# Optimization experiments

Measured on AMD Instinct MI355X. Metric: run time of the kernel, lower is better.

Reference implementation:

```python
import jax, jax.numpy as jnp
import numpy as np

B, S, D = 8, 2048, 1024
N = 256          # state_dim
H = 512          # selector_hidden
E = 8            # num_experts


def murmurhash3_finalizer(token_ids):
    # Torch code works in int64 but masks to 32 bits after each multiply and
    # values stay non-negative, so it is exactly uint32 wrapping arithmetic.
    x = token_ids.astype(jnp.uint32)
    x = x ^ (x >> 16)
    x = x * jnp.uint32(2246822507)
    x = x ^ (x >> 13)
    x = x * jnp.uint32(3266489909)
    x = x ^ (x >> 16)
    return x


def setup_inputs() -> dict:
    key = jax.random.key(0)
    ks = jax.random.split(key, 7)
    scale = 0.02
    return {
        "x": jax.random.normal(ks[0], (B, S, D), dtype=jnp.float32),
        "token_ids": jax.random.randint(ks[1], (B, S), 0, 50257, dtype=jnp.int32),
        "Win": jax.random.normal(ks[2], (E, N, D), dtype=jnp.float32) * scale,      # in_proj.weight per expert
        "Wsin": jax.random.normal(ks[3], (E, H, D), dtype=jnp.float32) * scale,     # selector_in.weight
        "Wsout": jax.random.normal(ks[4], (E, 4 * N, H), dtype=jnp.float32) * scale,  # selector_out.weight
        "Wout": jax.random.normal(ks[5], (E, D, N), dtype=jnp.float32) * scale,     # out_proj.weight
        "dparam": jnp.ones((E, N), dtype=jnp.float32),                              # per-expert d
    }


def _forward(x, Win, Wsin, Wsout, Wout, dparam, token_ids):
    b, s, d = x.shape
    e_num, n, _ = Win.shape
    routes = (murmurhash3_finalizer(token_ids) % jnp.uint32(e_num)).astype(jnp.int32)  # (B,S)

    # Per-token expert projections, selected by hash route (masked accumulation
    # over the small fixed expert count; honors per-token routing).
    u = jnp.zeros((b, s, n), x.dtype)
    a = jnp.zeros((b, s, n), x.dtype)
    bg = jnp.zeros((b, s, n), x.dtype)
    c = jnp.zeros((b, s, n), x.dtype)
    dg = jnp.zeros((b, s, n), x.dtype)
    for e in range(e_num):
        m = (routes == e)[..., None]
        u = jnp.where(m, jnp.einsum('bsd,nd->bsn', x, Win[e]), u)
        sh = jax.nn.silu(jnp.einsum('bsd,hd->bsh', x, Wsin[e]))
        sel = jnp.einsum('bsh,oh->bso', sh, Wsout[e])       # (B,S,4N)
        ar, br, cr, dr = jnp.split(sel, 4, axis=-1)
        a = jnp.where(m, jax.nn.sigmoid(ar), a)
        bg = jnp.where(m, jnp.tanh(br), bg)
        c = jnp.where(m, jnp.tanh(cr), c)
        dg = jnp.where(m, jax.nn.sigmoid(dr), dg)

    dvec = dparam[routes]              # (B,S,N) expert d param per token
    skip = dvec * dg * u               # residual term, state-independent

    bidx = jnp.arange(b)

    def step(states, inp):
        # states: (B,E,N) per-expert hidden state per batch row
        route_t, u_t, a_t, b_t, c_t, skip_t = inp
        h_prev = states[bidx, route_t]                 # (B,N)
        h = a_t * h_prev + b_t * u_t
        states = states.at[bidx, route_t].set(h)       # only routed expert updates
        y = c_t * h + skip_t
        return states, y

    xs = (routes.swapaxes(0, 1), u.swapaxes(0, 1), a.swapaxes(0, 1),
          bg.swapaxes(0, 1), c.swapaxes(0, 1), skip.swapaxes(0, 1))
    states0 = jnp.zeros((b, e_num, n), x.dtype)
    _, ys = jax.lax.scan(step, states0, xs)            # ys: (S,B,N)
    y = ys.swapaxes(0, 1)                              # (B,S,N)

    out = jnp.zeros((b, s, d), x.dtype)
    for e in range(e_num):
        m = (routes == e)[..., None]
        out = jnp.where(m, jnp.einsum('bsn,dn->bsd', y, Wout[e]), out)
    return out


def reference(x, token_ids, Win, Wsin, Wsout, Wout, dparam):
    return _forward(x, Win, Wsin, Wsout, Wout, dparam, token_ids)
```

## Files before the change

kernel.cpp:

```cpp
#include <hip/hip_runtime.h>


#define TOKS 16384
#define RPAD 16512
#define DD   1024
#define NN   256
#define HH   512
#define MAXTILES  136
#define MAXCHUNKS 576
#define CHUNK 32
#define CVTBLKS 12288

typedef short short8 __attribute__((ext_vector_type(8)));
typedef float floatx4 __attribute__((ext_vector_type(4)));
typedef _Float16 half_t;

#define AS_GLOBAL __attribute__((address_space(1)))
#define AS_LDS    __attribute__((address_space(3)))

__device__ __forceinline__ void gl_lds16(const void* g, void* l) {
    __builtin_amdgcn_global_load_lds((const AS_GLOBAL void*)g, (AS_LDS void*)l, 16, 0, 0);
}

__device__ __forceinline__ unsigned short f2bf(float f) {
    union { float f; unsigned u; } c; c.f = f;
    unsigned r = c.u + 0x7FFF + ((c.u >> 16) & 1);
    return (unsigned short)(r >> 16);
}
__device__ __forceinline__ int route_of(int token) {
    unsigned x = (unsigned)token;
    x ^= x >> 16; x *= 2246822507u; x ^= x >> 13; x *= 3266489909u; x ^= x >> 16;
    return (int)(x & 7u);
}
__device__ __forceinline__ float sigm(float v) { return 1.0f / (1.0f + __expf(-v)); }
__device__ __forceinline__ float ftanh(float v) {
    float e = __expf(2.0f * v);
    return 1.0f - 2.0f / (e + 1.0f);
}

__global__ void k_scatter(const int* __restrict__ tok,
                          int* __restrict__ perm,
                          int* __restrict__ tileE, int* __restrict__ tileS,
                          int* __restrict__ tileR,
                          int* __restrict__ cGrp, int* __restrict__ cStart,
                          int* __restrict__ cLen, int* __restrict__ gBase,
                          int* __restrict__ meta,
                          const float* __restrict__ Win, const float* __restrict__ Wsin,
                          const float* __restrict__ Wsout, const float* __restrict__ Wout,
                          unsigned short* __restrict__ W12, unsigned short* __restrict__ Wso,
                          unsigned short* __restrict__ Wo) {
    int blk = blockIdx.x, tid = threadIdx.x;
    if (blk >= 8) {
        const int C12 = 8 * 768 * 1024 / 4, CSO = 8 * 1024 * 512 / 4;
        int c = (blk - 8) * 256 + tid;
        floatx4 v; unsigned short* dst;
        if (c < C12) {
            int d = c * 4;
            int e = d / (768 * 1024);
            int rem = d - e * (768 * 1024);
            int r = rem >> 10, k = rem & 1023;
            const float* src = (r < 256) ? (Win + (((size_t)e * 256 + r) << 10) + k)
                                         : (Wsin + (((size_t)e * 512 + (r - 256)) << 10) + k);
            v = __builtin_nontemporal_load((const floatx4*)src);
            dst = W12 + d;
        } else if (c < C12 + CSO) {
            int d = (c - C12) * 4;
            v = __builtin_nontemporal_load((const floatx4*)(Wsout + d));
            dst = Wso + d;
        } else {
            int d = (c - C12 - CSO) * 4;
            v = __builtin_nontemporal_load((const floatx4*)(Wout + d));
            dst = Wo + d;
        }
        ushort4 o;
        o.x = f2bf(v[0]); o.y = f2bf(v[1]); o.z = f2bf(v[2]); o.w = f2bf(v[3]);
        *(ushort4*)dst = o;
        return;
    }
    int b = blk;
    int lane = tid & 63, w = tid >> 6;
    __shared__ int hh[8][8][32];
    __shared__ int sc[64], eoff[9], etile[9], gbs[65];
    __shared__ unsigned wsum[4][4];

    {
        int hr = tid >> 5, hs = tid & 31;
        const int* tp = tok + hr * 2048 + hs * 64;
        int hc[8] = {0,0,0,0,0,0,0,0};
        #pragma unroll 8
        for (int i = 0; i < 64; i++) hc[route_of(tp[i])]++;
        #pragma unroll
        for (int e = 0; e < 8; e++) hh[hr][e][hs] = hc[e];
    }
    int r[8];
    int myc[8] = {0,0,0,0,0,0,0,0};
    #pragma unroll
    for (int i = 0; i < 8; i++) {
        int e = route_of(tok[b * 2048 + tid * 8 + i]);
        r[i] = e; myc[e]++;
    }
    __syncthreads();
    if (tid < 64) {
        int row = tid >> 3, e = tid & 7, s = 0;
        #pragma unroll
        for (int s2 = 0; s2 < 32; s2++) s += hh[row][e][s2];
        sc[tid] = s;
    }
    __syncthreads();
    if (tid == 0) {
        int ce[8];
        for (int e = 0; e < 8; e++) {
            int s = 0;
            for (int b2 = 0; b2 < 8; b2++) s += sc[b2 * 8 + e];
            ce[e] = s;
        }
        eoff[0] = 0;
        for (int e = 0; e < 8; e++) eoff[e + 1] = eoff[e] + ce[e];
        if (b == 0) {
            etile[0] = 0;
            for (int e = 0; e < 8; e++) etile[e + 1] = etile[e] + (ce[e] + 127) / 128;
            meta[0] = etile[8];
            gbs[0] = 0;
            for (int g = 0; g < 64; g++) gbs[g + 1] = gbs[g] + (sc[g] + CHUNK - 1) / CHUNK;
            meta[1] = gbs[64];
        }
    }
    __syncthreads();
    unsigned p[4], v[4];
    #pragma unroll
    for (int k = 0; k < 4; k++) {
        p[k] = (unsigned)myc[2 * k] | ((unsigned)myc[2 * k + 1] << 16);
        v[k] = p[k];
    }
    #pragma unroll
    for (int off = 1; off < 64; off <<= 1) {
        #pragma unroll
        for (int k = 0; k < 4; k++) {
            unsigned o = __shfl_up(v[k], off, 64);
            if (lane >= off) v[k] += o;
        }
    }
    if (lane == 63) {
        #pragma unroll
        for (int k = 0; k < 4; k++) wsum[w][k] = v[k];
    }
    __syncthreads();
    unsigned add[4] = {0, 0, 0, 0};
    for (int ww = 0; ww < w; ww++)
        #pragma unroll
        for (int k = 0; k < 4; k++) add[k] += wsum[ww][k];
    int basep[8];
    #pragma unroll
    for (int e = 0; e < 8; e++) {
        int run = eoff[e];
        for (int b2 = 0; b2 < b; b2++) run += sc[b2 * 8 + e];
        unsigned ex = v[e >> 1] + add[e >> 1] - p[e >> 1];
        basep[e] = run + (int)((e & 1) ? (ex >> 16) : (ex & 0xffffu));
    }
    #pragma unroll
    for (int i = 0; i < 8; i++) {
        int e = r[i];
        perm[basep[e]++] = b * 2048 + tid * 8 + i;
    }
    if (b == 0) {
        if (tid < 8) {
            int e = tid, st = eoff[e], c = eoff[e + 1] - eoff[e], t0 = etile[e];
            for (int i = 0, k = 0; i < c; i += 128, k++) {
                tileE[t0 + k] = e; tileS[t0 + k] = st + i;
                tileR[t0 + k] = (c - i < 128) ? (c - i) : 128;
            }
        }
        if (tid < 64) {
            int g = tid, e = g & 7;
            int n = sc[g], base = gbs[g];
            int s0 = eoff[e];
            for (int b2 = 0; b2 < (g >> 3); b2++) s0 += sc[b2 * 8 + e];
            gBase[g] = base;
            for (int i = 0, c = 0; i < n; i += CHUNK, c++) {
                cGrp[base + c] = g;
                cStart[base + c] = s0 + i;
                cLen[base + c] = (n - i < CHUNK) ? (n - i) : CHUNK;
            }
        }
    }
}

__global__ void k_gather(const float* __restrict__ x, const int* __restrict__ perm,
                         unsigned short* __restrict__ Xs, unsigned short* __restrict__ SHb,
                         unsigned short* __restrict__ Yb) {
    int r = blockIdx.x, tid = threadIdx.x;
    if (r < TOKS) {
        int tok = perm[r];
        floatx4 v = __builtin_nontemporal_load(
            (const floatx4*)(x + (size_t)tok * 1024 + tid * 4));
        ushort4 o;
        o.x = f2bf(v[0]); o.y = f2bf(v[1]); o.z = f2bf(v[2]); o.w = f2bf(v[3]);
        *(ushort4*)(Xs + (size_t)r * 1024 + tid * 4) = o;
    } else {
        ushort4 z = {0, 0, 0, 0};
        *(ushort4*)(Xs + (size_t)r * 1024 + tid * 4) = z;
        if (tid < 128) *(ushort4*)(SHb + (size_t)r * 512 + tid * 4) = z;
        if (tid < 64)  *(ushort4*)(Yb + (size_t)r * 256 + tid * 4) = z;
    }
}

template<int MODE, int KD>
__global__ __launch_bounds__(256, 4)
void k_mfma(const unsigned short* __restrict__ A, const unsigned short* __restrict__ Bw,
            const int* __restrict__ perm, const float* __restrict__ dparam,
            half_t* __restrict__ Ub, unsigned short* __restrict__ SHb,
            half_t* __restrict__ Aa, half_t* __restrict__ Wg,
            half_t* __restrict__ Cc, half_t* __restrict__ Sk,
            float* __restrict__ out,
            const int* __restrict__ tileE, const int* __restrict__ tileS,
            const int* __restrict__ tileR, const int* __restrict__ meta) {
    const int mt = blockIdx.x;
    if (mt >= meta[0]) return;
    const int e = tileE[mt], pos0 = tileS[mt], rows = tileR[mt];
    const int col0 = blockIdx.y * 64;
    const int tid = threadIdx.x;
    const int w = tid >> 6, lane = tid & 63, quad = lane >> 4, l15 = lane & 15;
    const int wm = w & 1, wn = w >> 1;
    constexpr int NOUT = (MODE == 0) ? 768 : 1024;
    constexpr int NK = KD / 32;

    __shared__ unsigned short As[3][128 * 32];
    __shared__ unsigned short Bs[3][64 * 32];

    const int r0 = tid >> 2;
    const int c8s = ((tid & 3) ^ ((tid >> 3) & 3)) * 8;
    const unsigned short* ga = A + (size_t)(pos0 + r0) * KD + c8s;
    const unsigned short* gb = Bw + ((size_t)e * NOUT + col0 + r0) * KD + c8s;

    const int sq = (quad ^ ((l15 >> 1) & 3)) * 8;
    int aoff[4], boff[2];
    #pragma unroll
    for (int i = 0; i < 4; i++) aoff[i] = (wm * 64 + i * 16 + l15) * 32 + sq;
    #pragma unroll
    for (int j = 0; j < 2; j++) boff[j] = (wn * 32 + j * 16 + l15) * 32 + sq;

    floatx4 acc[4][2] = {};

    #define STAGE(buf, k0) do { \
        gl_lds16(ga + (k0),                    As[buf] + w * 512); \
        gl_lds16(ga + (size_t)64 * KD + (k0),  As[buf] + 2048 + w * 512); \
        gl_lds16(gb + (k0),                    Bs[buf] + w * 512); \
    } while (0)

    STAGE(0, 0);
    STAGE(1, 32);
    int cur = 0, pre = 2;
    for (int kt = 0; kt < NK; kt++) {
        if (kt < NK - 1) {
            asm volatile("s_waitcnt vmcnt(3)" ::: "memory");
        } else {
            asm volatile("s_waitcnt vmcnt(0)" ::: "memory");
        }
        __builtin_amdgcn_s_barrier();
        asm volatile("" ::: "memory");
        if (kt + 2 < NK) STAGE(pre, (kt + 2) * 32);
        short8 af[4], bf[2];
        #pragma unroll
        for (int i = 0; i < 4; i++) af[i] = *(const short8*)(As[cur] + aoff[i]);
        #pragma unroll
        for (int j = 0; j < 2; j++) bf[j] = *(const short8*)(Bs[cur] + boff[j]);
        __builtin_amdgcn_s_setprio(1);
        #pragma unroll
        for (int i = 0; i < 4; i++)
            #pragma unroll
            for (int j = 0; j < 2; j++)
                acc[i][j] = __builtin_amdgcn_mfma_f32_16x16x32_bf16(af[i], bf[j], acc[i][j], 0, 0, 0);
        __builtin_amdgcn_s_setprio(0);
        asm volatile("s_waitcnt lgkmcnt(0)" ::: "memory");
        __builtin_amdgcn_sched_barrier(0);
        cur = (cur == 2) ? 0 : cur + 1;
        pre = (pre == 2) ? 0 : pre + 1;
    }
    #undef STAGE
    asm volatile("" ::: "memory");

    #pragma unroll
    for (int i = 0; i < 4; i++) {
        #pragma unroll
        for (int r = 0; r < 4; r++) {
            int m = wm * 64 + i * 16 + quad * 4 + r;
            if (m >= rows) continue;
            size_t row = (size_t)(pos0 + m);
            if (MODE == 0) {
                if (col0 < 256) {
                    #pragma unroll
                    for (int j = 0; j < 2; j++) {
                        int n = col0 + wn * 32 + j * 16 + l15;
                        Ub[row * 256 + n] = (half_t)acc[i][j][r];
                    }
                } else {
                    #pragma unroll
                    for (int j = 0; j < 2; j++) {
                        int n = col0 - 256 + wn * 32 + j * 16 + l15;
                        float v = acc[i][j][r];
                        SHb[row * 512 + n] = f2bf(v * sigm(v));
                    }
                }
            } else if (MODE == 1) {
                int region = col0 >> 8;
                #pragma unroll
                for (int j = 0; j < 2; j++) {
                    int n0 = (col0 & 255) + wn * 32 + j * 16 + l15;
                    size_t idx = row * 256 + (size_t)n0;
                    float v = acc[i][j][r];
                    if (region == 0) {
                        Aa[idx] = (half_t)sigm(v);
                    } else if (region == 1) {
                        Wg[idx] = (half_t)(ftanh(v) * (float)Ub[idx]);
                    } else if (region == 2) {
                        Cc[idx] = (half_t)ftanh(v);
                    } else {
                        Sk[idx] = (half_t)(dparam[e * 256 + n0] * sigm(v) * (float)Ub[idx]);
                    }
                }
            } else {
                int tok = perm[row];
                #pragma unroll
                for (int j = 0; j < 2; j++) {
                    int n = col0 + wn * 32 + j * 16 + l15;
                    __builtin_nontemporal_store(acc[i][j][r], &out[(size_t)tok * 1024 + n]);
                }
            }
        }
    }
}

__global__ void k_scanA(const half_t* __restrict__ Aa, const half_t* __restrict__ Wg,
                        const int* __restrict__ cStart, const int* __restrict__ cLen,
                        const int* __restrict__ meta,
                        float* __restrict__ SA, float* __restrict__ SQ) {
    int id = blockIdx.x;
    if (id >= meta[1]) return;
    int t = threadIdx.x;
    int s0 = cStart[id], L = cLen[id];
    size_t idx = (size_t)s0 * 256 + t;
    float p = 1.0f, q = 0.0f;
    if (L == CHUNK) {
        #pragma unroll
        for (int i = 0; i < CHUNK; i++) {
            float a = (float)Aa[idx + (size_t)i * 256], ww = (float)Wg[idx + (size_t)i * 256];
            q = a * q + ww;
            p *= a;
        }
    } else {
        for (int i = 0; i < L; i++) {
            float a = (float)Aa[idx], ww = (float)Wg[idx];
            q = a * q + ww;
            p *= a;
            idx += 256;
        }
    }
    SA[(size_t)id * 256 + t] = p;
    SQ[(size_t)id * 256 + t] = q;
}

__global__ void k_scanC(const half_t* __restrict__ Aa, const half_t* __restrict__ Wg,
                        const half_t* __restrict__ Cc, const half_t* __restrict__ Sk,
                        const int* __restrict__ cGrp, const int* __restrict__ cStart,
                        const int* __restrict__ cLen, const int* __restrict__ gBase,
                        const float* __restrict__ SA, const float* __restrict__ SQ,
                        const int* __restrict__ meta,
                        unsigned short* __restrict__ Yb) {
    int id = blockIdx.x;
    if (id >= meta[1]) return;
    int t = threadIdx.x;
    int g = cGrp[id];
    int base = gBase[g];
    int c = id - base;
    float h = 0.0f;
    for (int j = 0; j < c; j++) {
        size_t k = (size_t)(base + j) * 256 + t;
        h = SA[k] * h + SQ[k];
    }
    int s0 = cStart[id], L = cLen[id];
    size_t idx = (size_t)s0 * 256 + t;
    if (L == CHUNK) {
        #pragma unroll
        for (int i = 0; i < CHUNK; i++) {
            size_t k = idx + (size_t)i * 256;
            float a = (float)Aa[k], ww = (float)Wg[k];
            float cc = (float)Cc[k], sk = (float)Sk[k];
            h = a * h + ww;
            Yb[k] = f2bf(cc * h + sk);
        }
    } else {
        for (int i = 0; i < L; i++) {
            float a = (float)Aa[idx], ww = (float)Wg[idx];
            float cc = (float)Cc[idx], sk = (float)Sk[idx];
            h = a * h + ww;
            Yb[idx] = f2bf(cc * h + sk);
            idx += 256;
        }
    }
}

extern "C" void kernel_launch(void* const* d_in, const int* in_sizes, int n_in,
                              void* d_out, int out_size, void* d_ws, size_t ws_size,
                              hipStream_t stream) {
    const float* xin   = (const float*)d_in[0];
    const int*   tok   = (const int*)d_in[1];
    const float* Win   = (const float*)d_in[2];
    const float* Wsin  = (const float*)d_in[3];
    const float* Wsout = (const float*)d_in[4];
    const float* Wout  = (const float*)d_in[5];
    const float* dpar  = (const float*)d_in[6];
    float* out = (float*)d_out;

    size_t off = 0;
    char* base = (char*)d_ws;
    auto alloc = [&](size_t bytes) -> void* {
        void* p = base + off;
        off += (bytes + 255) & ~(size_t)255;
        return p;
    };
    half_t*         Ub  = (half_t*)alloc((size_t)RPAD * NN * 2);
    unsigned short* SHb = (unsigned short*)alloc((size_t)RPAD * HH * 2);
    unsigned short* Xs  = (unsigned short*)alloc((size_t)RPAD * DD * 2);
    unsigned short* Yb  = (unsigned short*)alloc((size_t)RPAD * NN * 2);
    half_t* Aa = (half_t*)alloc((size_t)TOKS * NN * 2);
    half_t* Wg = (half_t*)alloc((size_t)TOKS * NN * 2);
    half_t* Cc = (half_t*)alloc((size_t)TOKS * NN * 2);
    half_t* Sk = (half_t*)alloc((size_t)TOKS * NN * 2);
    unsigned short* W12 = (unsigned short*)alloc((size_t)8 * 768 * 1024 * 2);
    unsigned short* Wso = (unsigned short*)alloc((size_t)8 * 1024 * 512 * 2);
    unsigned short* Wo  = (unsigned short*)alloc((size_t)8 * 1024 * 256 * 2);
    float* SA  = (float*)alloc((size_t)MAXCHUNKS * 256 * 4);
    float* SQ  = (float*)alloc((size_t)MAXCHUNKS * 256 * 4);
    int* perm   = (int*)alloc(TOKS * 4);
    int* tileE  = (int*)alloc(MAXTILES * 4);
    int* tileS  = (int*)alloc(MAXTILES * 4);
    int* tileR  = (int*)alloc(MAXTILES * 4);
    int* cGrp   = (int*)alloc(MAXCHUNKS * 4);
    int* cStart = (int*)alloc(MAXCHUNKS * 4);
    int* cLen   = (int*)alloc(MAXCHUNKS * 4);
    int* gBase  = (int*)alloc(64 * 4);
    int* meta   = (int*)alloc(16 * 4);

    k_scatter<<<8 + CVTBLKS, 256, 0, stream>>>(tok, perm, tileE, tileS, tileR,
                                               cGrp, cStart, cLen, gBase, meta,
                                               Win, Wsin, Wsout, Wout, W12, Wso, Wo);
    k_gather<<<RPAD, 256, 0, stream>>>(xin, perm, Xs, SHb, Yb);

    k_mfma<0, 1024><<<dim3(MAXTILES, 12), 256, 0, stream>>>(Xs, W12, perm, dpar,
        Ub, SHb, Aa, Wg, Cc, Sk, out, tileE, tileS, tileR, meta);
    k_mfma<1, 512><<<dim3(MAXTILES, 16), 256, 0, stream>>>(SHb, Wso, perm, dpar,
        Ub, SHb, Aa, Wg, Cc, Sk, out, tileE, tileS, tileR, meta);

    k_scanA<<<MAXCHUNKS, 256, 0, stream>>>(Aa, Wg, cStart, cLen, meta, SA, SQ);
    k_scanC<<<MAXCHUNKS, 256, 0, stream>>>(Aa, Wg, Cc, Sk, cGrp, cStart, cLen,
                                           gBase, SA, SQ, meta, Yb);

    k_mfma<2, 256><<<dim3(MAXTILES, 16), 256, 0, stream>>>(Yb, Wo, perm, dpar,
        Ub, SHb, Aa, Wg, Cc, Sk, out, tileE, tileS, tileR, meta);
}
```

Measured before the change: 317.8 us.

## Give each wave private LDS staging to drop block barriers in GEMM loop

Each wave now loads its own A (64 rows) and B (32 rows) slices into a private triple-buffered LDS region, so the per-iteration block-wide s_barrier is removed and waves run independently. The cost is duplicated global loads: A rows are loaded by both wn waves and B rows by both wm waves, which doubles LDS footprint (72KB) and halves occupancy via launch_bounds(256,2). It trades barrier stalls for more memory traffic and fewer resident blocks.

```diff
diff --git a/kernel.cpp b/kernel.cpp
--- a/kernel.cpp
+++ b/kernel.cpp
@@ -205,7 +205,7 @@
 }
 
 template<int MODE, int KD>
-__global__ __launch_bounds__(256, 4)
+__global__ __launch_bounds__(256, 2)
 void k_mfma(const unsigned short* __restrict__ A, const unsigned short* __restrict__ Bw,
             const int* __restrict__ perm, const float* __restrict__ dparam,
             half_t* __restrict__ Ub, unsigned short* __restrict__ SHb,
@@ -224,27 +224,29 @@
     constexpr int NOUT = (MODE == 0) ? 768 : 1024;
     constexpr int NK = KD / 32;
 
-    __shared__ unsigned short As[3][128 * 32];
-    __shared__ unsigned short Bs[3][64 * 32];
-
-    const int r0 = tid >> 2;
-    const int c8s = ((tid & 3) ^ ((tid >> 3) & 3)) * 8;
-    const unsigned short* ga = A + (size_t)(pos0 + r0) * KD + c8s;
-    const unsigned short* gb = Bw + ((size_t)e * NOUT + col0 + r0) * KD + c8s;
+    __shared__ unsigned short WS[4][3][3072];
+
+    const int c8w = ((lane & 3) ^ ((lane >> 3) & 3)) * 8;
+    const unsigned short* gaw = A + (size_t)(pos0 + wm * 64 + (lane >> 2)) * KD + c8w;
+    const unsigned short* gbw = Bw + ((size_t)e * NOUT + col0 + wn * 32 + (lane >> 2)) * KD + c8w;
 
     const int sq = (quad ^ ((l15 >> 1) & 3)) * 8;
     int aoff[4], boff[2];
     #pragma unroll
-    for (int i = 0; i < 4; i++) aoff[i] = (wm * 64 + i * 16 + l15) * 32 + sq;
-    #pragma unroll
-    for (int j = 0; j < 2; j++) boff[j] = (wn * 32 + j * 16 + l15) * 32 + sq;
+    for (int i = 0; i < 4; i++) aoff[i] = (i * 16 + l15) * 32 + sq;
+    #pragma unroll
+    for (int j = 0; j < 2; j++) boff[j] = 2048 + (j * 16 + l15) * 32 + sq;
 
     floatx4 acc[4][2] = {};
 
     #define STAGE(buf, k0) do { \
-        gl_lds16(ga + (k0),                    As[buf] + w * 512); \
-        gl_lds16(ga + (size_t)64 * KD + (k0),  As[buf] + 2048 + w * 512); \
-        gl_lds16(gb + (k0),                    Bs[buf] + w * 512); \
+        unsigned short* dst_ = &WS[w][buf][0]; \
+        gl_lds16(gaw + (k0),                     dst_); \
+        gl_lds16(gaw + (size_t)16 * KD + (k0),   dst_ + 512); \
+        gl_lds16(gaw + (size_t)32 * KD + (k0),   dst_ + 1024); \
+        gl_lds16(gaw + (size_t)48 * KD + (k0),   dst_ + 1536); \
+        gl_lds16(gbw + (k0),                     dst_ + 2048); \
+        gl_lds16(gbw + (size_t)16 * KD + (k0),   dst_ + 2560); \
     } while (0)
 
     STAGE(0, 0);
@@ -252,18 +254,17 @@
     int cur = 0, pre = 2;
     for (int kt = 0; kt < NK; kt++) {
         if (kt < NK - 1) {
-            asm volatile("s_waitcnt vmcnt(3)" ::: "memory");
+            asm volatile("s_waitcnt vmcnt(6)" ::: "memory");
         } else {
             asm volatile("s_waitcnt vmcnt(0)" ::: "memory");
         }
-        __builtin_amdgcn_s_barrier();
-        asm volatile("" ::: "memory");
         if (kt + 2 < NK) STAGE(pre, (kt + 2) * 32);
+        const unsigned short* sb = &WS[w][cur][0];
         short8 af[4], bf[2];
         #pragma unroll
-        for (int i = 0; i < 4; i++) af[i] = *(const short8*)(As[cur] + aoff[i]);
-        #pragma unroll
-        for (int j = 0; j < 2; j++) bf[j] = *(const short8*)(Bs[cur] + boff[j]);
+        for (int i = 0; i < 4; i++) af[i] = *(const short8*)(sb + aoff[i]);
+        #pragma unroll
+        for (int j = 0; j < 2; j++) bf[j] = *(const short8*)(sb + boff[j]);
         __builtin_amdgcn_s_setprio(1);
         #pragma unroll
         for (int i = 0; i < 4; i++)
@@ -277,7 +278,6 @@
         pre = (pre == 2) ? 0 : pre + 1;
     }
     #undef STAGE
-    asm volatile("" ::: "memory");
 
     #pragma unroll
     for (int i = 0; i < 4; i++) {
```

New measurement: 361.0 us. +13.6%, slower.
